# Kernel optimization log

Hardware: AMD Instinct MI355X
Metric: run time of the kernel (lower is better)

## Reference

```python
import jax, jax.numpy as jnp
import numpy as np

N = 100000   # nodes
E = 1600000  # edges (before self-loops)
DIN, DH, DL = 128, 128, 64


def setup_inputs() -> dict:
    key = jax.random.key(0)
    ks = jax.random.split(key, 6)
    feat = jax.random.normal(ks[0], (N, DIN), dtype=jnp.float32)
    src = jax.random.randint(ks[1], (E,), 0, N)
    dst = jax.random.randint(ks[2], (E,), 0, N)

    def glorot(k, i, o):
        return jax.random.normal(k, (i, o), dtype=jnp.float32) * (1.0 / np.sqrt(i))

    return dict(
        feat=feat, src=src, dst=dst,
        W1=glorot(ks[3], DIN, DH), b1=jnp.zeros((DH,), jnp.float32),
        W2=glorot(ks[4], DH, DH), b2=jnp.zeros((DH,), jnp.float32),
        W3=glorot(ks[5], DH, DL), b3=jnp.zeros((DL,), jnp.float32),
    )


def _graph_conv(feat, src, dst, out_isqrt, in_isqrt, W, b):
    # DGL GraphConv, norm='both': scale src by d_out^{-1/2}, sum messages
    # into dst, scale by d_in^{-1/2}, then dense transform.
    h = feat * out_isqrt[:, None]                                   # [N, F]
    agg = jax.ops.segment_sum(h[src], dst, num_segments=N)          # [N, F]
    agg = agg * in_isqrt[:, None]
    return agg @ W + b


def reference(feat, src, dst, W1, b1, W2, b2, W3, b3):
    # dgl.add_self_loop: append (i, i) for every node
    loops = jnp.arange(N, dtype=src.dtype)
    s = jnp.concatenate([src, loops])
    d = jnp.concatenate([dst, loops])

    ones = jnp.ones(s.shape[0], dtype=feat.dtype)
    deg_out = jax.ops.segment_sum(ones, s, num_segments=N)
    deg_in = jax.ops.segment_sum(ones, d, num_segments=N)
    out_isqrt = jax.lax.rsqrt(jnp.maximum(deg_out, 1.0))
    in_isqrt = jax.lax.rsqrt(jnp.maximum(deg_in, 1.0))

    h = jax.nn.relu(_graph_conv(feat, s, d, out_isqrt, in_isqrt, W1, b1))
    h = jax.nn.relu(_graph_conv(h, s, d, out_isqrt, in_isqrt, W2, b2))
    return _graph_conv(h, s, d, out_isqrt, in_isqrt, W3, b3)
```

## Files before the change

kernel.cpp:

```cpp
#include <hip/hip_runtime.h>
#include <hip/hip_fp16.h>

#define NN 100000
#define NE 1600000
#define KDIM 128

#define BSH 8
#define NBKT ((NN + 255) >> BSH)
#define BCAP 6144
#define CHUNK 4096
#define CPAD 16

#define SRC_MASK 0x1FFFFu

#define CVT_BLOCKS (NN * KDIM / 8 / 256)

typedef _Float16 half8 __attribute__((ext_vector_type(8)));
typedef float f32x4 __attribute__((ext_vector_type(4)));

template <int NOUT>
__device__ inline void packW_body(const float* __restrict__ W, _Float16* __restrict__ Wp,
                                  int blk) {
    constexpr int NT = NOUT / 16;
    int idx = blk * 256 + threadIdx.x;
    if (idx >= 128 * NOUT) return;
    int j = idx & 7;
    int l = (idx >> 3) & 63;
    int rest = idx >> 9;
    int nt = rest % NT;
    int kt = rest / NT;
    int k = kt * 32 + ((l >> 4) & 3) * 8 + j;
    int n = nt * 16 + (l & 15);
    Wp[idx] = (_Float16)W[(size_t)k * NOUT + n];
}

__global__ __launch_bounds__(256) void k_prep(const float* __restrict__ W1,
                                              const float* __restrict__ W2,
                                              const float* __restrict__ W3,
                                              _Float16* __restrict__ Wp1,
                                              _Float16* __restrict__ Wp2,
                                              _Float16* __restrict__ Wp3,
                                              unsigned* __restrict__ cursor_d,
                                              unsigned* __restrict__ cursor_s,
                                              const float* __restrict__ f,
                                              __half* __restrict__ o) {
    int b = blockIdx.x;
    if (b < 64) packW_body<128>(W1, Wp1, b);
    else if (b < 128) packW_body<128>(W2, Wp2, b - 64);
    else if (b < 160) packW_body<64>(W3, Wp3, b - 128);
    else if (b == 160) {
        for (int k = threadIdx.x; k < NBKT; k += 256) {
            cursor_d[(size_t)k * CPAD] = (unsigned)k * BCAP;
            cursor_s[(size_t)k * CPAD] = (unsigned)k * BCAP;
        }
    } else {
        int i = (b - 161) * 256 + threadIdx.x;
        if (i < NN * KDIM / 8) {
            const float4* f4 = (const float4*)f + 2 * (size_t)i;
            float4 a = f4[0], bb = f4[1];
            __half2 h0 = __floats2half2_rn(a.x, a.y);
            __half2 h1 = __floats2half2_rn(a.z, a.w);
            __half2 h2 = __floats2half2_rn(bb.x, bb.y);
            __half2 h3 = __floats2half2_rn(bb.z, bb.w);
            __half2 hh[4] = {h0, h1, h2, h3};
            *((uint4*)o + i) = *(uint4*)hh;
        }
    }
}

__global__ __launch_bounds__(512) void k_part2(const int* __restrict__ src,
                                               const int* __restrict__ dst,
                                               unsigned* __restrict__ cursor_d,
                                               unsigned* __restrict__ cursor_s,
                                               unsigned* __restrict__ part_d,
                                               unsigned char* __restrict__ part_s) {
    __shared__ unsigned histd[NBKT];
    __shared__ unsigned hists[NBKT];
    __shared__ unsigned lofsd[NBKT], lofss[NBKT];
    __shared__ unsigned gbased[NBKT], gbases[NBKT];
    __shared__ unsigned sbuf[512];
    __shared__ unsigned staged[CHUNK];
    __shared__ unsigned short stagebd[CHUNK];
    __shared__ unsigned char stages[CHUNK];
    __shared__ unsigned short stagebs[CHUNK];

    const int e0 = blockIdx.x * CHUNK;
    const int lim = min(CHUNK, NE - e0);
    const int t = threadIdx.x;

    for (int k = t; k < NBKT; k += 512) {
        histd[k] = 0u;
        hists[k] = 0u;
    }
    __syncthreads();

    unsigned es[CHUNK / 512], ed[CHUNK / 512];
    int nmine = 0;
#pragma unroll
    for (int i = 0; i < CHUNK / 512; ++i) {
        int r = t + i * 512;
        if (r < lim) {
            es[i] = (unsigned)src[e0 + r];
            ed[i] = (unsigned)dst[e0 + r];
            atomicAdd(&histd[ed[i] >> BSH], 1u);
            atomicAdd(&hists[es[i] >> BSH], 1u);
            nmine = i + 1;
        }
    }
    __syncthreads();

    unsigned vd = (t < NBKT) ? histd[t] : 0u;
    unsigned vs = (t < NBKT) ? hists[t] : 0u;
    unsigned v = (vd << 16) | vs;
    sbuf[t] = v;
    __syncthreads();
    for (int off = 1; off < 512; off <<= 1) {
        unsigned x = sbuf[t];
        if (t >= off) x += sbuf[t - off];
        __syncthreads();
        sbuf[t] = x;
        __syncthreads();
    }
    if (t < NBKT) {
        unsigned ld = (sbuf[t] >> 16) - vd;
        unsigned ls = (sbuf[t] & 0xFFFFu) - vs;
        lofsd[t] = ld;
        lofss[t] = ls;
        gbased[t] = (vd ? atomicAdd(&cursor_d[(size_t)t * CPAD], vd) : 0u) - ld;
        gbases[t] = (vs ? atomicAdd(&cursor_s[(size_t)t * CPAD], vs) : 0u) - ls;
        histd[t] = 0u;
        hists[t] = 0u;
    }
    __syncthreads();

#pragma unroll
    for (int i = 0; i < CHUNK / 512; ++i) {
        if (i < nmine) {
            unsigned kd = ed[i] >> BSH;
            unsigned pd = lofsd[kd] + atomicAdd(&histd[kd], 1u);
            staged[pd] = es[i] | ((ed[i] & 255u) << 17);
            stagebd[pd] = (unsigned short)kd;
            unsigned ks = es[i] >> BSH;
            unsigned ps = lofss[ks] + atomicAdd(&hists[ks], 1u);
            stages[ps] = (unsigned char)(es[i] & 255u);
            stagebs[ps] = (unsigned short)ks;
        }
    }
    __syncthreads();

    for (int j = t; j < lim; j += 512) {
        unsigned k = stagebd[j];
        unsigned gaddr = gbased[k] + (unsigned)j;
        if (gaddr - k * BCAP < BCAP)
            part_d[gaddr] = staged[j];
        unsigned k2 = stagebs[j];
        unsigned gaddr2 = gbases[k2] + (unsigned)j;
        if (gaddr2 - k2 * BCAP < BCAP)
            part_s[gaddr2] = stages[j];
    }
}

__global__ __launch_bounds__(256) void k_build(const unsigned* __restrict__ cursor_d,
                                               const unsigned* __restrict__ cursor_s,
                                               const unsigned* __restrict__ part_d,
                                               const unsigned char* __restrict__ part_s,
                                               unsigned* __restrict__ cnt_in,
                                               float* __restrict__ oi,
                                               float* __restrict__ ii,
                                               unsigned* __restrict__ row_start,
                                               unsigned* __restrict__ csr) {
    __shared__ unsigned c[256];
    __shared__ unsigned c2[256];
    __shared__ unsigned s[256];
    __shared__ unsigned red[256];
    __shared__ unsigned cur[256];
    __shared__ unsigned stage[BCAP];
    const int b = blockIdx.x;
    const int t = threadIdx.x;

    unsigned ps = 0;
    for (int k = t; k < b; k += 256)
        ps += min(cursor_d[(size_t)k * CPAD] - (unsigned)k * BCAP, (unsigned)BCAP);
    red[t] = ps;
    c[t] = 0u;
    c2[t] = 0u;
    __syncthreads();
    for (int off = 128; off > 0; off >>= 1) {
        if (t < off) red[t] += red[t + off];
        __syncthreads();
    }
    const unsigned prefix = red[0];

    unsigned cntd = min(cursor_d[(size_t)b * CPAD] - (unsigned)b * BCAP, (unsigned)BCAP);
    unsigned cnts = min(cursor_s[(size_t)b * CPAD] - (unsigned)b * BCAP, (unsigned)BCAP);
    const unsigned* ppd = part_d + (size_t)b * BCAP;
    const unsigned char* pps = part_s + (size_t)b * BCAP;
    for (unsigned j = t; j < cntd; j += 256)
        atomicAdd(&c[(ppd[j] >> 17) & 255u], 1u);
    for (unsigned j = t; j < cnts; j += 256)
        atomicAdd(&c2[pps[j]], 1u);
    __syncthreads();

    unsigned v = c[t];
    s[t] = v;
    __syncthreads();
    for (int off = 1; off < 256; off <<= 1) {
        unsigned x = s[t];
        if (t >= off) x += s[t - off];
        __syncthreads();
        s[t] = x;
        __syncthreads();
    }
    int node = (b << BSH) + t;
    if (node < NN) {
        cnt_in[node] = v;
        ii[node] = rsqrtf((float)(v + 1u));
        oi[node] = rsqrtf((float)(c2[t] + 1u));
        row_start[node] = prefix + s[t] - v;
    }
    cur[t] = s[t] - v;
    __syncthreads();

    for (unsigned j = t; j < cntd; j += 256) {
        unsigned e = ppd[j];
        unsigned p = atomicAdd(&cur[(e >> 17) & 255u], 1u);
        stage[p] = e & SRC_MASK;
    }
    __syncthreads();
    for (unsigned j = t; j < cntd; j += 256)
        csr[prefix + j] = stage[j];
}

template <bool SCALE_SRC>
__global__ __launch_bounds__(256) void k_agg128h(const __half* __restrict__ h,
                                                 const float* __restrict__ oi,
                                                 const float* __restrict__ ii,
                                                 const unsigned* __restrict__ row_start,
                                                 const unsigned* __restrict__ cnt_in,
                                                 const unsigned* __restrict__ csr,
                                                 __half* __restrict__ out) {
    int wid = (int)((blockIdx.x * 256u + threadIdx.x) >> 6);
    int lane = threadIdx.x & 63;
    if (wid >= NN) return;
    const __half2* hv = (const __half2*)h;
    float2 acc;
    {
        float2 v = __half22float2(hv[(size_t)wid * 64 + lane]);
        float sc = SCALE_SRC ? oi[wid] : 1.f;
        acc.x = v.x * sc;
        acc.y = v.y * sc;
    }
    unsigned rs = row_start[wid];
    unsigned nk = cnt_in[wid];
    for (unsigned base = 0; base < nk; base += 64) {
        unsigned m = min(64u, nk - base);
        unsigned myidx = ((unsigned)lane < m) ? csr[rs + base + lane] : 0u;
        unsigned k = 0;
        for (; k + 16 <= m; k += 16) {
            unsigned s[16];
            float sc[16];
            __half2 v[16];
#pragma unroll
            for (int i = 0; i < 16; ++i) {
                s[i] = (unsigned)__builtin_amdgcn_readlane((int)myidx, (int)(k + i));
                v[i] = hv[(size_t)s[i] * 64 + lane];
                if (SCALE_SRC) sc[i] = oi[s[i]];
            }
#pragma unroll
            for (int i = 0; i < 16; ++i) {
                float2 f = __half22float2(v[i]);
                if (SCALE_SRC) {
                    acc.x = fmaf(f.x, sc[i], acc.x);
                    acc.y = fmaf(f.y, sc[i], acc.y);
                } else {
                    acc.x += f.x;
                    acc.y += f.y;
                }
            }
        }
        if (k < m) {
            unsigned s[16];
            float sc[16];
            __half2 v[16];
#pragma unroll
            for (int i = 0; i < 16; ++i) {
                s[i] = (unsigned)__builtin_amdgcn_readlane((int)myidx, (int)(k + i));
                v[i] = hv[(size_t)s[i] * 64 + lane];
                float w = SCALE_SRC ? oi[s[i]] : 1.f;
                sc[i] = (k + i < m) ? w : 0.f;
            }
#pragma unroll
            for (int i = 0; i < 16; ++i) {
                float2 f = __half22float2(v[i]);
                acc.x = fmaf(f.x, sc[i], acc.x);
                acc.y = fmaf(f.y, sc[i], acc.y);
            }
        }
    }
    float si = ii[wid];
    ((__half2*)out)[(size_t)wid * 64 + lane] = __floats2half2_rn(acc.x * si, acc.y * si);
}

__global__ __launch_bounds__(256) void k_agg64h(const __half* __restrict__ t,
                                                const float* __restrict__ ii,
                                                const float* __restrict__ bias,
                                                const unsigned* __restrict__ row_start,
                                                const unsigned* __restrict__ cnt_in,
                                                const unsigned* __restrict__ csr,
                                                float* __restrict__ out) {
    int wid = (int)((blockIdx.x * 256u + threadIdx.x) >> 6);
    int lane = threadIdx.x & 63;
    if (wid >= NN) return;
    float acc = __half2float(t[(size_t)wid * 64 + lane]);
    unsigned rs = row_start[wid];
    unsigned nk = cnt_in[wid];
    for (unsigned base = 0; base < nk; base += 64) {
        unsigned m = min(64u, nk - base);
        unsigned myidx = ((unsigned)lane < m) ? csr[rs + base + lane] : 0u;
        unsigned k = 0;
        for (; k + 16 <= m; k += 16) {
            unsigned s[16];
            __half v[16];
#pragma unroll
            for (int i = 0; i < 16; ++i) {
                s[i] = (unsigned)__builtin_amdgcn_readlane((int)myidx, (int)(k + i));
                v[i] = t[(size_t)s[i] * 64 + lane];
            }
#pragma unroll
            for (int i = 0; i < 16; ++i) acc += __half2float(v[i]);
        }
        if (k < m) {
            unsigned s[16];
            float sc[16];
            __half v[16];
#pragma unroll
            for (int i = 0; i < 16; ++i) {
                s[i] = (unsigned)__builtin_amdgcn_readlane((int)myidx, (int)(k + i));
                v[i] = t[(size_t)s[i] * 64 + lane];
                sc[i] = (k + i < m) ? 1.f : 0.f;
            }
#pragma unroll
            for (int i = 0; i < 16; ++i) acc = fmaf(__half2float(v[i]), sc[i], acc);
        }
    }
    out[(size_t)wid * 64 + lane] = acc * ii[wid] + bias[lane];
}

__global__ __launch_bounds__(256) void k_gemm1(const _Float16* __restrict__ A,
                                               const _Float16* __restrict__ Wp,
                                               const float* __restrict__ bias,
                                               const float* __restrict__ oscale,
                                               _Float16* __restrict__ Y16) {
    constexpr int NT = 8;
    const int w = threadIdx.x >> 6;
    const int l = threadIdx.x & 63;
    const int r0 = blockIdx.x * 128 + w * 32;
    int arow0 = r0 + (l & 15);
    int arow1 = arow0 + 16;
    if (arow0 >= NN) arow0 = NN - 1;
    if (arow1 >= NN) arow1 = NN - 1;
    const half8* Ap0 = (const half8*)(A + (size_t)arow0 * 128) + (l >> 4);
    const half8* Ap1 = (const half8*)(A + (size_t)arow1 * 128) + (l >> 4);
    const half8* Bp = (const half8*)Wp + l;

    f32x4 acc0[NT], acc1[NT];
#pragma unroll
    for (int n = 0; n < NT; ++n) {
        acc0[n] = {0.f, 0.f, 0.f, 0.f};
        acc1[n] = {0.f, 0.f, 0.f, 0.f};
    }
#pragma unroll
    for (int kt = 0; kt < 4; ++kt) {
        half8 a0 = Ap0[kt * 4];
        half8 a1 = Ap1[kt * 4];
#pragma unroll
        for (int n = 0; n < NT; ++n) {
            half8 b = Bp[(kt * NT + n) * 64];
            acc0[n] = __builtin_amdgcn_mfma_f32_16x16x32_f16(a0, b, acc0[n], 0, 0, 0);
            acc1[n] = __builtin_amdgcn_mfma_f32_16x16x32_f16(a1, b, acc1[n], 0, 0, 0);
        }
    }
    const int col = l & 15;
#pragma unroll
    for (int half = 0; half < 2; ++half) {
        const int rbase = r0 + half * 16 + (l >> 4) * 4;
        f32x4* acc = half ? acc1 : acc0;
#pragma unroll
        for (int j = 0; j < 4; ++j) {
            int row = rbase + j;
            if (row >= NN) continue;
            float os = oscale[row];
#pragma unroll
            for (int n = 0; n < NT; ++n) {
                float v = fmaxf(acc[n][j] + bias[n * 16 + col], 0.f);
                Y16[(size_t)row * 128 + n * 16 + col] = (_Float16)(v * os);
            }
        }
    }
}

__global__ __launch_bounds__(256) void k_gemm23(const _Float16* __restrict__ A,
                                                const _Float16* __restrict__ Wp2,
                                                const _Float16* __restrict__ Wp3,
                                                const float* __restrict__ bias,
                                                const float* __restrict__ oscale,
                                                _Float16* __restrict__ T16) {
    constexpr int NT = 8;
    __shared__ _Float16 As[4][16][136];
    const int w = threadIdx.x >> 6;
    const int l = threadIdx.x & 63;
    const int r0 = blockIdx.x * 64 + w * 16;
    int arow = r0 + (l & 15);
    if (arow >= NN) arow = NN - 1;
    const half8* Ap = (const half8*)(A + (size_t)arow * 128) + (l >> 4);
    const half8* Bp2 = (const half8*)Wp2 + l;
    const half8* Bp3 = (const half8*)Wp3 + l;

    f32x4 acc[NT];
#pragma unroll
    for (int n = 0; n < NT; ++n) acc[n] = {0.f, 0.f, 0.f, 0.f};
#pragma unroll
    for (int kt = 0; kt < 4; ++kt) {
        half8 a = Ap[kt * 4];
#pragma unroll
        for (int n = 0; n < NT; ++n) {
            half8 b = Bp2[(kt * NT + n) * 64];
            acc[n] = __builtin_amdgcn_mfma_f32_16x16x32_f16(a, b, acc[n], 0, 0, 0);
        }
    }

    const int col = l & 15;
    const int rloc = (l >> 4) * 4;
#pragma unroll
    for (int j = 0; j < 4; ++j) {
        int row = r0 + rloc + j;
        float os = (row < NN) ? oscale[row] : 0.f;
#pragma unroll
        for (int n = 0; n < NT; ++n) {
            float v = fmaxf(acc[n][j] + bias[n * 16 + col], 0.f);
            As[w][rloc + j][n * 16 + col] = (_Float16)(v * os);
        }
    }

    f32x4 acc2[4];
#pragma unroll
    for (int n = 0; n < 4; ++n) acc2[n] = {0.f, 0.f, 0.f, 0.f};
    const int fr = l & 15;
    const int fg = l >> 4;
#pragma unroll
    for (int kt = 0; kt < 4; ++kt) {
        half8 a = *(const half8*)&As[w][fr][kt * 32 + fg * 8];
#pragma unroll
        for (int n = 0; n < 4; ++n) {
            half8 b = Bp3[(kt * 4 + n) * 64];
            acc2[n] = __builtin_amdgcn_mfma_f32_16x16x32_f16(a, b, acc2[n], 0, 0, 0);
        }
    }
#pragma unroll
    for (int j = 0; j < 4; ++j) {
        int row = r0 + rloc + j;
        if (row >= NN) continue;
#pragma unroll
        for (int n = 0; n < 4; ++n)
            T16[(size_t)row * 64 + n * 16 + col] = (_Float16)acc2[n][j];
    }
}

extern "C" void kernel_launch(void* const* d_in, const int* in_sizes, int n_in,
                              void* d_out, int out_size, void* d_ws, size_t ws_size,
                              hipStream_t stream) {
    const float* feat = (const float*)d_in[0];
    const int* src = (const int*)d_in[1];
    const int* dst = (const int*)d_in[2];
    const float* W1 = (const float*)d_in[3];
    const float* b1 = (const float*)d_in[4];
    const float* W2 = (const float*)d_in[5];
    const float* b2 = (const float*)d_in[6];
    const float* W3 = (const float*)d_in[7];
    const float* b3 = (const float*)d_in[8];
    float* out = (float*)d_out;

    char* p = (char*)d_ws;
    auto take = [&](size_t bytes) {
        char* q = p;
        p += (bytes + 255) & ~(size_t)255;
        return q;
    };
    unsigned* cnt_in = (unsigned*)take((size_t)NN * 4);
    float* oi = (float*)take((size_t)NN * 4);
    float* ii = (float*)take((size_t)NN * 4);
    unsigned* row_start = (unsigned*)take((size_t)NN * 4);
    unsigned* cursor_d = (unsigned*)take((size_t)NBKT * CPAD * 4);
    unsigned* cursor_s = (unsigned*)take((size_t)NBKT * CPAD * 4);
    unsigned* csr = (unsigned*)take((size_t)NE * 4);
    unsigned char* part_s = (unsigned char*)take((size_t)NBKT * BCAP);
    __half* feat16 = (__half*)take((size_t)NN * KDIM * 2);
    __half* H16 = (__half*)take((size_t)NN * KDIM * 2);
    __half* G16 = (__half*)take((size_t)NN * KDIM * 2);
    _Float16* Wp1 = (_Float16*)take((size_t)128 * 128 * 2);
    _Float16* Wp2 = (_Float16*)take((size_t)128 * 128 * 2);
    _Float16* Wp3 = (_Float16*)take((size_t)128 * 64 * 2);
    char* regionB = take((size_t)NN * 64 * 2 > (size_t)NBKT * BCAP * 4
                             ? (size_t)NN * 64 * 2
                             : (size_t)NBKT * BCAP * 4);
    unsigned* part_d = (unsigned*)regionB;
    __half* T16 = (__half*)regionB;

    k_prep<<<161 + CVT_BLOCKS, 256, 0, stream>>>(W1, W2, W3, Wp1, Wp2, Wp3, cursor_d,
                                                 cursor_s, feat, feat16);
    k_part2<<<(NE + CHUNK - 1) / CHUNK, 512, 0, stream>>>(src, dst, cursor_d, cursor_s,
                                                          part_d, part_s);
    k_build<<<NBKT, 256, 0, stream>>>(cursor_d, cursor_s, part_d, part_s, cnt_in, oi, ii,
                                      row_start, csr);

    const int AGG_BLOCKS = (NN + 3) / 4;
    const int GEMM1_BLOCKS = (NN + 127) / 128;
    const int GEMM23_BLOCKS = (NN + 63) / 64;

    k_agg128h<true><<<AGG_BLOCKS, 256, 0, stream>>>(feat16, oi, ii, row_start, cnt_in, csr, G16);
    k_gemm1<<<GEMM1_BLOCKS, 256, 0, stream>>>((const _Float16*)G16, Wp1, b1, oi,
                                              (_Float16*)H16);
    k_agg128h<false><<<AGG_BLOCKS, 256, 0, stream>>>(H16, oi, ii, row_start, cnt_in, csr, G16);
    k_gemm23<<<GEMM23_BLOCKS, 256, 0, stream>>>((const _Float16*)G16, Wp2, Wp3, b2, oi,
                                                (_Float16*)T16);
    k_agg64h<<<AGG_BLOCKS, 256, 0, stream>>>(T16, ii, b3, row_start, cnt_in, csr, out);
}
```

Baseline: 271.8 us.

## Use wave-shuffle scans, halve partition chunk, add 8-wide aggregation tail

```diff
diff --git a/kernel.cpp b/kernel.cpp
--- a/kernel.cpp
+++ b/kernel.cpp
@@ -8,7 +8,7 @@
 #define BSH 8
 #define NBKT ((NN + 255) >> BSH)
 #define BCAP 6144
-#define CHUNK 4096
+#define CHUNK 2048
 #define CPAD 16
 
 #define SRC_MASK 0x1FFFFu
@@ -78,7 +78,7 @@
     __shared__ unsigned hists[NBKT];
     __shared__ unsigned lofsd[NBKT], lofss[NBKT];
     __shared__ unsigned gbased[NBKT], gbases[NBKT];
-    __shared__ unsigned sbuf[512];
+    __shared__ unsigned wsum[8];
     __shared__ unsigned staged[CHUNK];
     __shared__ unsigned short stagebd[CHUNK];
     __shared__ unsigned char stages[CHUNK];
@@ -87,6 +87,8 @@
     const int e0 = blockIdx.x * CHUNK;
     const int lim = min(CHUNK, NE - e0);
     const int t = threadIdx.x;
+    const int lane = t & 63;
+    const int wv = t >> 6;
 
     for (int k = t; k < NBKT; k += 512) {
         histd[k] = 0u;
@@ -112,18 +114,29 @@
     unsigned vd = (t < NBKT) ? histd[t] : 0u;
     unsigned vs = (t < NBKT) ? hists[t] : 0u;
     unsigned v = (vd << 16) | vs;
-    sbuf[t] = v;
-    __syncthreads();
-    for (int off = 1; off < 512; off <<= 1) {
-        unsigned x = sbuf[t];
-        if (t >= off) x += sbuf[t - off];
-        __syncthreads();
-        sbuf[t] = x;
-        __syncthreads();
-    }
+    unsigned x = v;
+#pragma unroll
+    for (int off = 1; off < 64; off <<= 1) {
+        unsigned y = __shfl_up(x, off);
+        if (lane >= off) x += y;
+    }
+    if (lane == 63) wsum[wv] = x;
+    __syncthreads();
+    if (wv == 0) {
+        unsigned z = (lane < 8) ? wsum[lane] : 0u;
+#pragma unroll
+        for (int off = 1; off < 8; off <<= 1) {
+            unsigned y = __shfl_up(z, off);
+            if (lane >= off) z += y;
+        }
+        if (lane < 8) wsum[lane] = z;
+    }
+    __syncthreads();
+    unsigned incl = x + (wv ? wsum[wv - 1] : 0u);
+
     if (t < NBKT) {
-        unsigned ld = (sbuf[t] >> 16) - vd;
-        unsigned ls = (sbuf[t] & 0xFFFFu) - vs;
+        unsigned ld = (incl >> 16) - vd;
+        unsigned ls = (incl & 0xFFFFu) - vs;
         lofsd[t] = ld;
         lofss[t] = ls;
         gbased[t] = (vd ? atomicAdd(&cursor_d[(size_t)t * CPAD], vd) : 0u) - ld;
@@ -171,25 +184,24 @@
                                                unsigned* __restrict__ csr) {
     __shared__ unsigned c[256];
     __shared__ unsigned c2[256];
-    __shared__ unsigned s[256];
-    __shared__ unsigned red[256];
+    __shared__ unsigned wsum[4];
     __shared__ unsigned cur[256];
     __shared__ unsigned stage[BCAP];
     const int b = blockIdx.x;
     const int t = threadIdx.x;
+    const int lane = t & 63;
+    const int wv = t >> 6;
 
     unsigned ps = 0;
     for (int k = t; k < b; k += 256)
         ps += min(cursor_d[(size_t)k * CPAD] - (unsigned)k * BCAP, (unsigned)BCAP);
-    red[t] = ps;
+#pragma unroll
+    for (int off = 32; off > 0; off >>= 1) ps += __shfl_xor(ps, off);
+    if (lane == 0) wsum[wv] = ps;
     c[t] = 0u;
     c2[t] = 0u;
     __syncthreads();
-    for (int off = 128; off > 0; off >>= 1) {
-        if (t < off) red[t] += red[t + off];
-        __syncthreads();
-    }
-    const unsigned prefix = red[0];
+    const unsigned prefix = wsum[0] + wsum[1] + wsum[2] + wsum[3];
 
     unsigned cntd = min(cursor_d[(size_t)b * CPAD] - (unsigned)b * BCAP, (unsigned)BCAP);
     unsigned cnts = min(cursor_s[(size_t)b * CPAD] - (unsigned)b * BCAP, (unsigned)BCAP);
@@ -202,23 +214,34 @@
     __syncthreads();
 
     unsigned v = c[t];
-    s[t] = v;
-    __syncthreads();
-    for (int off = 1; off < 256; off <<= 1) {
-        unsigned x = s[t];
-        if (t >= off) x += s[t - off];
-        __syncthreads();
-        s[t] = x;
-        __syncthreads();
-    }
+    unsigned x = v;
+#pragma unroll
+    for (int off = 1; off < 64; off <<= 1) {
+        unsigned y = __shfl_up(x, off);
+        if (lane >= off) x += y;
+    }
+    if (lane == 63) wsum[wv] = x;
+    __syncthreads();
+    if (wv == 0) {
+        unsigned z = (lane < 4) ? wsum[lane] : 0u;
+#pragma unroll
+        for (int off = 1; off < 4; off <<= 1) {
+            unsigned y = __shfl_up(z, off);
+            if (lane >= off) z += y;
+        }
+        if (lane < 4) wsum[lane] = z;
+    }
+    __syncthreads();
+    unsigned incl = x + (wv ? wsum[wv - 1] : 0u);
+
     int node = (b << BSH) + t;
     if (node < NN) {
         cnt_in[node] = v;
         ii[node] = rsqrtf((float)(v + 1u));
         oi[node] = rsqrtf((float)(c2[t] + 1u));
-        row_start[node] = prefix + s[t] - v;
-    }
-    cur[t] = s[t] - v;
+        row_start[node] = prefix + incl - v;
+    }
+    cur[t] = incl - v;
     __syncthreads();
 
     for (unsigned j = t; j < cntd; j += 256) {
@@ -278,7 +301,8 @@
                 }
             }
         }
-        if (k < m) {
+        unsigned rem = m - k;
+        if (rem > 8) {
             unsigned s[16];
             float sc[16];
             __half2 v[16];
@@ -291,6 +315,23 @@
             }
 #pragma unroll
             for (int i = 0; i < 16; ++i) {
+                float2 f = __half22float2(v[i]);
+                acc.x = fmaf(f.x, sc[i], acc.x);
+                acc.y = fmaf(f.y, sc[i], acc.y);
+            }
+        } else if (rem) {
+            unsigned s[8];
+            float sc[8];
+            __half2 v[8];
+#pragma unroll
+            for (int i = 0; i < 8; ++i) {
+                s[i] = (unsigned)__builtin_amdgcn_readlane((int)myidx, (int)(k + i));
+                v[i] = hv[(size_t)s[i] * 64 + lane];
+                float w = SCALE_SRC ? oi[s[i]] : 1.f;
+                sc[i] = (k + i < m) ? w : 0.f;
+            }
+#pragma unroll
+            for (int i = 0; i < 8; ++i) {
                 float2 f = __half22float2(v[i]);
                 acc.x = fmaf(f.x, sc[i], acc.x);
                 acc.y = fmaf(f.y, sc[i], acc.y);
@@ -329,7 +370,8 @@
 #pragma unroll
             for (int i = 0; i < 16; ++i) acc += __half2float(v[i]);
         }
-        if (k < m) {
+        unsigned rem = m - k;
+        if (rem > 8) {
             unsigned s[16];
             float sc[16];
             __half v[16];
@@ -341,6 +383,18 @@
             }
 #pragma unroll
             for (int i = 0; i < 16; ++i) acc = fmaf(__half2float(v[i]), sc[i], acc);
+        } else if (rem) {
+            unsigned s[8];
+            float sc[8];
+            __half v[8];
+#pragma unroll
+            for (int i = 0; i < 8; ++i) {
+                s[i] = (unsigned)__builtin_amdgcn_readlane((int)myidx, (int)(k + i));
+                v[i] = t[(size_t)s[i] * 64 + lane];
+                sc[i] = (k + i < m) ? 1.f : 0.f;
+            }
+#pragma unroll
+            for (int i = 0; i < 8; ++i) acc = fmaf(__half2float(v[i]), sc[i], acc);
         }
     }
     out[(size_t)wid * 64 + lane] = acc * ii[wid] + bias[lane];
```

After: 282.2 us. +3.8%, slower.
